# Performance work log

Measured on AMD Instinct MI355X. Metric: run time of the kernel, lower is better.

Reference implementation:

```python
import jax, jax.numpy as jnp
import numpy as np

# per-item cutpoint counts (from np.unique(item_positions, return_counts=True))
NUM_CUTS = np.array([4, 5, 6, 7] * 4)  # 16 items
N_ITEMS = len(NUM_CUTS)
MAX_CP = int(NUM_CUTS.max())  # 7
CP = jnp.asarray(NUM_CUTS)  # [I]
CUT_MASK = jnp.arange(MAX_CP)[None, :] < CP[:, None]  # [I, MAX_CP] valid cutpoints
EPS = 1e-8

B, D_IN, H1, H2 = 65536, 512, 1024, 512


def setup_inputs() -> dict:
    key = jax.random.key(0)
    ks = jax.random.split(key, 10)
    x = jax.random.normal(ks[0], (B, D_IN), dtype=jnp.float32)
    data = jax.random.randint(ks[1], (B, N_ITEMS), 0, 4, dtype=jnp.int64 if jax.config.jax_enable_x64 else jnp.int32)
    W1 = jax.random.normal(ks[2], (D_IN, H1), dtype=jnp.float32) / np.sqrt(D_IN)
    b1 = jnp.zeros((H1,), jnp.float32)
    W2 = jax.random.normal(ks[3], (H1, H2), dtype=jnp.float32) / np.sqrt(H1)
    b2 = jnp.zeros((H2,), jnp.float32)
    Wf = jax.random.normal(ks[4], (H2, N_ITEMS), dtype=jnp.float32) / np.sqrt(H2)
    bf = jnp.zeros((N_ITEMS,), jnp.float32)
    # ragged per-item cutpoint heads padded to MAX_CP (masked in reference)
    Wk = jax.random.normal(ks[5], (N_ITEMS, H2, MAX_CP), dtype=jnp.float32) / np.sqrt(H2)
    bk = jnp.zeros((N_ITEMS, MAX_CP), jnp.float32)
    return {"x": x, "data": data, "W1": W1, "b1": b1, "W2": W2, "b2": b2,
            "Wf": Wf, "bf": bf, "Wk": Wk, "bk": bk}


def reference(x, data, W1, b1, W2, b2, Wf, bf, Wk, bk):
    # trunk MLP: Linear -> ReLU, twice
    h = jax.nn.relu(x @ W1 + b1)
    h = jax.nn.relu(h @ W2 + b2)  # [B, H2]
    f_x = h @ Wf + bf  # [B, I]
    # batched ragged per-item cutpoint heads (padded GEMM + mask)
    cut = jnp.einsum('bh,ihc->bic', h, Wk) + bk  # [B, I, MAX_CP]
    e = jnp.where(CUT_MASK[None], jnp.clip(jnp.exp(cut), EPS, None), 0.0)
    cum = jnp.cumsum(e, axis=-1)  # monotone cutpoints; pads contribute 0
    cum_probs = jnp.clip(jax.nn.sigmoid(cum - f_x[:, :, None]), EPS, 1.0 - EPS)
    # category probs: [cum0, diffs..., 1 - cum_last], ragged lengths cp_i + 1
    diff = jnp.concatenate([cum_probs[..., :1], cum_probs[..., 1:] - cum_probs[..., :-1]], axis=-1)
    last_cum = cum_probs[:, jnp.arange(N_ITEMS), CP - 1]  # [B, I]
    diff_pad = jnp.pad(diff, ((0, 0), (0, 0), (0, 1)))  # [B, I, MAX_CP+1]
    cat = jnp.arange(MAX_CP + 1)[None, None, :]
    probs = jnp.where(cat < CP[None, :, None], diff_pad,
                      jnp.where(cat == CP[None, :, None], (1.0 - last_cum)[:, :, None], 1.0))
    probs = jnp.clip(probs, EPS, 1.0 - EPS)  # [B, I, MAX_CP+1]
    # NLL: gather observed category per (respondent, item)
    gathered = jnp.take_along_axis(probs, data[:, :, None].astype(jnp.int32), axis=2)[..., 0]
    rec_loss = -jnp.log(gathered).mean(axis=0).sum()
    return rec_loss, probs
```

## Files before the change

### kernel.cpp

```cpp
#include <hip/hip_runtime.h>
#include <cmath>

#define EPSV 1e-8f

typedef __bf16 bf16_t;
typedef __bf16 bf16x8 __attribute__((ext_vector_type(8)));
typedef __bf16 bf16x4 __attribute__((ext_vector_type(4)));
typedef float f32x4 __attribute__((ext_vector_type(4)));

__device__ __forceinline__ void gload16(const void* g, void* l) {
    __builtin_amdgcn_global_load_lds(
        (const __attribute__((address_space(1))) void*)g,
        (__attribute__((address_space(3))) void*)l, 16, 0, 0);
}

__device__ __forceinline__ void qmap(int q, int& row, int& u) {
    int prow = q >> 3;
    int v = (q & 7) ^ (prow & 7);
    row = (prow << 1) | (v >> 2);
    u = v & 3;
}
__device__ __forceinline__ int lds_elem(int row, int u) {
    int prow = row >> 1;
    int v = ((row & 1) << 2) | u;
    return prow * 64 + ((v ^ (prow & 7)) << 3);
}

template<bool RELU>
__global__ __launch_bounds__(512, 2) void gemm256(
    const bf16_t* __restrict__ A, const bf16_t* __restrict__ BT,
    const float* __restrict__ bias, bf16_t* __restrict__ C,
    int N, int K, int nbx)
{
    __shared__ bf16_t sm[2][2][2][8192];

    const int t    = threadIdx.x;
    const int lane = t & 63;
    const int w    = t >> 6;
    const int wr   = w >> 2;
    const int wc   = w & 3;
    const int r16  = lane & 15;
    const int u16  = lane >> 4;

    const int nwg = gridDim.x;
    int bid = blockIdx.x;
    int swz = ((nwg & 7) == 0) ? ((bid & 7) * (nwg >> 3) + (bid >> 3)) : bid;
    const int bx = swz % nbx, by = swz / nbx;
    const int m0 = by << 8, n0 = bx << 8;

    int r0, u0, r1, u1;
    qmap(t, r0, u0);
    qmap(t + 512, r1, u1);
    const bf16_t* gA0 = A  + (size_t)(m0 + r0) * K + (u0 << 3);
    const bf16_t* gA1 = A  + (size_t)(m0 + r1) * K + (u1 << 3);
    const bf16_t* gB0 = BT + (size_t)(n0 + r0) * K + (u0 << 3);
    const bf16_t* gB1 = BT + (size_t)(n0 + r1) * K + (u1 << 3);

    auto STAGE = [&](const bf16_t* g0, const bf16_t* g1, bf16_t* sl, int koff) {
        gload16(g0 + koff, sl + (w << 9));
        gload16(g1 + koff, sl + 4096 + (w << 9));
    };

    int aoff[8], boff[4];
#pragma unroll
    for (int i = 0; i < 8; ++i) aoff[i] = lds_elem((wr << 7) + (i << 4) + r16, u16);
#pragma unroll
    for (int j = 0; j < 4; ++j) boff[j] = lds_elem((wc << 6) + (j << 4) + r16, u16);

    f32x4 acc[8][4];
#pragma unroll
    for (int i = 0; i < 8; ++i)
#pragma unroll
        for (int j = 0; j < 4; ++j) acc[i][j] = (f32x4){0.f, 0.f, 0.f, 0.f};

    const int NT = K >> 6;

    STAGE(gA0, gA1, &sm[0][0][0][0], 0);
    STAGE(gB0, gB1, &sm[0][1][0][0], 0);
    STAGE(gA0, gA1, &sm[0][0][1][0], 32);
    STAGE(gB0, gB1, &sm[0][1][1][0], 32);
    STAGE(gA0, gA1, &sm[1][0][0][0], 64);
    STAGE(gB0, gB1, &sm[1][1][0][0], 64);
    asm volatile("s_waitcnt vmcnt(8)" ::: "memory");
    __builtin_amdgcn_s_barrier();

    bf16x8 af0[4], af1[4], bfr[4];
#pragma unroll
    for (int i = 0; i < 4; ++i) af0[i] = *(const bf16x8*)(&sm[0][0][0][0] + aoff[i]);

    for (int kt = 0; kt < NT; ++kt) {
        const int c  = kt & 1;
        const int c1 = c ^ 1;
        const bool s12 = (kt + 1) < NT;
        const bool s34 = (kt + 2) < NT;
        const int k12 = ((kt + 1) << 6) + 32;
        const int k34 = (kt + 2) << 6;
        const bf16_t* sA0 = &sm[c][0][0][0];
        const bf16_t* sA1 = &sm[c][0][1][0];
        const bf16_t* sB0 = &sm[c][1][0][0];
        const bf16_t* sB1 = &sm[c][1][1][0];

#pragma unroll
        for (int j = 0; j < 4; ++j) bfr[j] = *(const bf16x8*)(sB0 + boff[j]);
#pragma unroll
        for (int i = 0; i < 4; ++i) af1[i] = *(const bf16x8*)(sA0 + aoff[4 + i]);
        if (s12) STAGE(gA0, gA1, &sm[c1][0][1][0], k12);
        __builtin_amdgcn_s_barrier();
        __builtin_amdgcn_s_setprio(1);
#pragma unroll
        for (int i = 0; i < 4; ++i)
#pragma unroll
            for (int j = 0; j < 4; ++j)
                acc[i][j] = __builtin_amdgcn_mfma_f32_16x16x32_bf16(bfr[j], af0[i], acc[i][j], 0, 0, 0);
        __builtin_amdgcn_s_setprio(0);
        __builtin_amdgcn_s_barrier();

        if (s12) STAGE(gB0, gB1, &sm[c1][1][1][0], k12);
        if (s12) asm volatile("s_waitcnt vmcnt(8)" ::: "memory");
        else     asm volatile("s_waitcnt vmcnt(0)" ::: "memory");
        __builtin_amdgcn_s_barrier();
#pragma unroll
        for (int i = 0; i < 4; ++i) af0[i] = *(const bf16x8*)(sA1 + aoff[i]);
        __builtin_amdgcn_s_setprio(1);
#pragma unroll
        for (int i = 0; i < 4; ++i)
#pragma unroll
            for (int j = 0; j < 4; ++j)
                acc[4 + i][j] = __builtin_amdgcn_mfma_f32_16x16x32_bf16(bfr[j], af1[i], acc[4 + i][j], 0, 0, 0);
        __builtin_amdgcn_s_setprio(0);
        __builtin_amdgcn_s_barrier();

#pragma unroll
        for (int j = 0; j < 4; ++j) bfr[j] = *(const bf16x8*)(sB1 + boff[j]);
#pragma unroll
        for (int i = 0; i < 4; ++i) af1[i] = *(const bf16x8*)(sA1 + aoff[4 + i]);
        if (s34) STAGE(gA0, gA1, &sm[c][0][0][0], k34);
        __builtin_amdgcn_s_barrier();
        __builtin_amdgcn_s_setprio(1);
#pragma unroll
        for (int i = 0; i < 4; ++i)
#pragma unroll
            for (int j = 0; j < 4; ++j)
                acc[i][j] = __builtin_amdgcn_mfma_f32_16x16x32_bf16(bfr[j], af0[i], acc[i][j], 0, 0, 0);
        __builtin_amdgcn_s_setprio(0);
        __builtin_amdgcn_s_barrier();

        if (s34) STAGE(gB0, gB1, &sm[c][1][0][0], k34);
        if (s34)      asm volatile("s_waitcnt vmcnt(8)" ::: "memory");
        else if (s12) asm volatile("s_waitcnt vmcnt(4)" ::: "memory");
        __builtin_amdgcn_s_barrier();
        if (s12) {
#pragma unroll
            for (int i = 0; i < 4; ++i)
                af0[i] = *(const bf16x8*)(&sm[c1][0][0][0] + aoff[i]);
        }
        __builtin_amdgcn_s_setprio(1);
#pragma unroll
        for (int i = 0; i < 4; ++i)
#pragma unroll
            for (int j = 0; j < 4; ++j)
                acc[4 + i][j] = __builtin_amdgcn_mfma_f32_16x16x32_bf16(bfr[j], af1[i], acc[4 + i][j], 0, 0, 0);
        __builtin_amdgcn_s_setprio(0);
        __builtin_amdgcn_s_barrier();
    }

    __syncthreads();

    char* eb = (char*)&sm[0][0][0][0];
    const int mBb = (wr << 7) + r16;
    const int nBb = (wc << 6) + (u16 << 2);
#pragma unroll
    for (int i = 0; i < 8; ++i) {
        const int m = mBb + (i << 4);
        const int xm = (m & 15) << 4;
#pragma unroll
        for (int j = 0; j < 4; ++j) {
            const int nl = nBb + (j << 4);
            f32x4 bv = *(const f32x4*)(bias + n0 + nl);
            bf16x4 pk;
#pragma unroll
            for (int r = 0; r < 4; ++r) {
                float v = acc[i][j][r] + bv[r];
                if (RELU) v = fmaxf(v, 0.f);
                pk[r] = (bf16_t)v;
            }
            *(bf16x4*)(eb + m * 512 + ((nl << 1) ^ xm)) = pk;
        }
    }
    __syncthreads();
    const int cc = t & 31;
    const int rr = t >> 5;
#pragma unroll
    for (int rp = 0; rp < 16; ++rp) {
        const int m = (rp << 4) + rr;
        bf16x8 v = *(const bf16x8*)(eb + m * 512 + (((cc << 4) ^ ((m & 15) << 4)) & 511));
        *(bf16x8*)(C + (size_t)(m0 + m) * N + n0 + (cc << 3)) = v;
    }
}

__global__ __launch_bounds__(256) void head_fused(
    const bf16_t* __restrict__ A, const bf16_t* __restrict__ BT,
    const float* __restrict__ bias, const int* __restrict__ data,
    float* __restrict__ probs_out, float* __restrict__ partials,
    int K, int row0)
{
    __shared__ __align__(16) bf16_t As[128 * 32];
    __shared__ __align__(16) bf16_t Bs[128 * 32];
    __shared__ float hdl[128 * 128];

    const int t    = threadIdx.x;
    const int lane = t & 63;
    const int w    = t >> 6;
    const int wm   = (w >> 1) << 6;
    const int wn   = (w & 1) << 6;
    const int m0l  = blockIdx.x << 7;

    const int srow  = t >> 2;
    const int skoff = (t & 3) << 3;

    const bf16_t* Ap = A  + (size_t)(m0l + srow) * K + skoff;
    const bf16_t* Bp = BT + (size_t)srow * K + skoff;
    const size_t rstep = (size_t)64 * K;

    bf16_t* lA0 = As + ((w << 6)      ) * 8;
    bf16_t* lA1 = As + ((w << 6) + 256) * 8;
    bf16_t* lB0 = Bs + ((w << 6)      ) * 8;
    bf16_t* lB1 = Bs + ((w << 6) + 256) * 8;

    f32x4 acc[4][4];
#pragma unroll
    for (int i = 0; i < 4; ++i)
#pragma unroll
        for (int j = 0; j < 4; ++j) acc[i][j] = (f32x4){0.f, 0.f, 0.f, 0.f};

    const int r16  = lane & 15;
    const int u16  = lane >> 4;
    const int kblk = u16 << 3;

    for (int k0 = 0; k0 < K; k0 += 32) {
        __syncthreads();
        gload16(Ap + k0,         lA0);
        gload16(Ap + rstep + k0, lA1);
        gload16(Bp + k0,         lB0);
        gload16(Bp + rstep + k0, lB1);
        __syncthreads();

        bf16x8 af[4], bfr[4];
#pragma unroll
        for (int i = 0; i < 4; ++i) {
            af[i]  = *(const bf16x8*)&As[(wm + (i << 4) + r16) * 32 + kblk];
            bfr[i] = *(const bf16x8*)&Bs[(wn + (i << 4) + r16) * 32 + kblk];
        }
#pragma unroll
        for (int i = 0; i < 4; ++i)
#pragma unroll
            for (int j = 0; j < 4; ++j)
                acc[i][j] = __builtin_amdgcn_mfma_f32_16x16x32_bf16(af[i], bfr[j], acc[i][j], 0, 0, 0);
    }

#pragma unroll
    for (int j = 0; j < 4; ++j) {
        const int col = wn + (j << 4) + r16;
        const float bv = bias[col];
#pragma unroll
        for (int i = 0; i < 4; ++i) {
            const int rb = wm + (i << 4) + (u16 << 2);
#pragma unroll
            for (int r = 0; r < 4; ++r)
                hdl[(rb + r) * 128 + col] = acc[i][j][r] + bv;
        }
    }
    __syncthreads();

    float lsum = 0.f;
    const int item = t & 15;
    const int cp   = 4 + (item & 3);
#pragma unroll
    for (int p = 0; p < 8; ++p) {
        const int row = (p << 4) + (t >> 4);
        const float* h = hdl + row * 128;
        const size_t grow = (size_t)row0 + m0l + row;

        const float f = h[item];
        float cumP[7];
        float cum = 0.f;
#pragma unroll
        for (int c = 0; c < 7; ++c) {
            if (c < cp) {
                float e = fmaxf(expf(h[16 + item * 7 + c]), EPSV);
                cum += e;
                float s = 1.f / (1.f + expf(f - cum));
                cumP[c] = fminf(fmaxf(s, EPSV), 1.f - EPSV);
            } else {
                cumP[c] = 0.f;
            }
        }
        float probs[8];
#pragma unroll
        for (int k = 0; k < 8; ++k) {
            float v;
            if (k < cp)       v = (k == 0) ? cumP[0] : (cumP[k] - cumP[k - 1]);
            else if (k == cp) v = 1.f - cumP[cp - 1];
            else              v = 1.f;
            probs[k] = fminf(fmaxf(v, EPSV), 1.f - EPSV);
        }
        float* dst = probs_out + (grow * 16 + item) * 8;
#pragma unroll
        for (int k = 0; k < 8; ++k) dst[k] = probs[k];

        const int d = data[grow * 16 + item];
        float g = probs[0];
#pragma unroll
        for (int k = 1; k < 8; ++k) g = (d == k) ? probs[k] : g;
        lsum += -logf(g);
    }

    __syncthreads();
    float* red = (float*)As;
    red[t] = lsum;
    __syncthreads();
#pragma unroll
    for (int s2 = 128; s2 > 0; s2 >>= 1) {
        if (t < s2) red[t] += red[t + s2];
        __syncthreads();
    }
    if (t == 0) partials[(row0 >> 7) + blockIdx.x] = red[0];
}

__global__ __launch_bounds__(256) void convert_x(
    const float* __restrict__ in, bf16_t* __restrict__ out, int n8)
{
    int i = blockIdx.x * 256 + threadIdx.x;
    if (i >= n8) return;
    const float4* p = (const float4*)in;
    float4 a = p[2 * i], b = p[2 * i + 1];
    bf16x8 v;
    v[0] = (bf16_t)a.x; v[1] = (bf16_t)a.y; v[2] = (bf16_t)a.z; v[3] = (bf16_t)a.w;
    v[4] = (bf16_t)b.x; v[5] = (bf16_t)b.y; v[6] = (bf16_t)b.z; v[7] = (bf16_t)b.w;
    ((bf16x8*)out)[i] = v;
}

__global__ __launch_bounds__(256) void transpose_w(
    const float* __restrict__ in, bf16_t* __restrict__ out,
    int kshift, int N, int total)
{
    int idx = blockIdx.x * 256 + threadIdx.x;
    if (idx >= total) return;
    int n = idx >> kshift;
    int k = idx & ((1 << kshift) - 1);
    out[idx] = (bf16_t)in[(size_t)k * N + n];
}

__global__ __launch_bounds__(256) void pack_head(
    const float* __restrict__ Wf, const float* __restrict__ bfv,
    const float* __restrict__ Wk, const float* __restrict__ bk,
    bf16_t* __restrict__ WhT, float* __restrict__ bhead)
{
    int idx = blockIdx.x * 256 + threadIdx.x;
    int n = idx >> 9;
    int k = idx & 511;
    float v;
    if (n < 16) {
        v = Wf[k * 16 + n];
    } else {
        int m = n - 16;
        int i = m / 7, c = m % 7;
        v = Wk[(size_t)i * 3584 + (size_t)k * 7 + c];
    }
    WhT[idx] = (bf16_t)v;
    if (idx < 128) bhead[idx] = (idx < 16) ? bfv[idx] : bk[idx - 16];
}

__global__ __launch_bounds__(256) void reduce_loss(
    const float* __restrict__ partials, int n, float* __restrict__ out, float scale)
{
    __shared__ float red[256];
    float s = 0.f;
    for (int i = threadIdx.x; i < n; i += 256) s += partials[i];
    red[threadIdx.x] = s;
    __syncthreads();
    for (int k = 128; k > 0; k >>= 1) {
        if (threadIdx.x < k) red[threadIdx.x] += red[threadIdx.x + k];
        __syncthreads();
    }
    if (threadIdx.x == 0) out[0] = red[0] * scale;
}

extern "C" void kernel_launch(void* const* d_in, const int* in_sizes, int n_in,
                              void* d_out, int out_size, void* d_ws, size_t ws_size,
                              hipStream_t stream)
{
    const float* x   = (const float*)d_in[0];
    const int*   dat = (const int*)d_in[1];
    const float* W1  = (const float*)d_in[2];
    const float* b1  = (const float*)d_in[3];
    const float* W2  = (const float*)d_in[4];
    const float* b2  = (const float*)d_in[5];
    const float* Wf  = (const float*)d_in[6];
    const float* bfv = (const float*)d_in[7];
    const float* Wk  = (const float*)d_in[8];
    const float* bk  = (const float*)d_in[9];
    float* out = (float*)d_out;

    const int B = 65536, DIN = 512, H1 = 1024, H2 = 512;

    char* cur = (char*)d_ws;
    auto carve = [&](size_t bytes) {
        char* p = cur;
        cur += (bytes + 255) & ~(size_t)255;
        return p;
    };
    float*  partials = (float*)carve(4096 * 4);
    float*  bhead    = (float*)carve(512);
    bf16_t* W1T      = (bf16_t*)carve((size_t)H1 * DIN * 2);
    bf16_t* W2T      = (bf16_t*)carve((size_t)H2 * H1 * 2);
    bf16_t* WhT      = (bf16_t*)carve((size_t)128 * H2 * 2);

    size_t used = (size_t)(cur - (char*)d_ws);
    size_t avail = (ws_size > used + 1024) ? (ws_size - used - 1024) : 0;
    int SLICE = 2048;
    const int cands[6] = {65536, 32768, 16384, 8192, 4096, 2048};
    for (int ci = 0; ci < 6; ++ci) {
        if ((size_t)cands[ci] * 4096 <= avail) { SLICE = cands[ci]; break; }
    }
    bf16_t* xb = (bf16_t*)carve((size_t)SLICE * DIN * 2);
    bf16_t* h1 = (bf16_t*)carve((size_t)SLICE * H1 * 2);
    bf16_t* h2 = (bf16_t*)carve((size_t)SLICE * H2 * 2);

    transpose_w<<<(H1 * DIN + 255) / 256, 256, 0, stream>>>(W1, W1T, 9,  H1, H1 * DIN);
    transpose_w<<<(H2 * H1 + 255) / 256, 256, 0, stream>>>(W2, W2T, 10, H2, H2 * H1);
    pack_head<<<256, 256, 0, stream>>>(Wf, bfv, Wk, bk, WhT, bhead);

    for (int r0 = 0; r0 < B; r0 += SLICE) {
        convert_x<<<SLICE / 4, 256, 0, stream>>>(x + (size_t)r0 * DIN, xb, SLICE * DIN / 8);
        gemm256<true><<<(SLICE / 256) * (H1 / 256), 512, 0, stream>>>(xb, W1T, b1, h1, H1, DIN, H1 / 256);
        gemm256<true><<<(SLICE / 256) * (H2 / 256), 512, 0, stream>>>(h1, W2T, b2, h2, H2, H1, H2 / 256);
        head_fused<<<SLICE / 128, 256, 0, stream>>>(h2, WhT, bhead, dat, out + 1, partials, H2, r0);
    }
    reduce_loss<<<1, 256, 0, stream>>>(partials, B / 128, out, 1.0f / B);
}
```

Before: 237.5 us.

## Use simpler 128x128 single-buffered GEMM kernel for first layer

```diff
diff --git a/kernel.cpp b/kernel.cpp
--- a/kernel.cpp
+++ b/kernel.cpp
@@ -12,6 +12,103 @@
     __builtin_amdgcn_global_load_lds(
         (const __attribute__((address_space(1))) void*)g,
         (__attribute__((address_space(3))) void*)l, 16, 0, 0);
+}
+
+template<bool RELU>
+__global__ __launch_bounds__(256) void gemm128(
+    const bf16_t* __restrict__ A, const bf16_t* __restrict__ BT,
+    const float* __restrict__ bias, bf16_t* __restrict__ C,
+    int N, int K, int nbx)
+{
+    __shared__ __align__(16) bf16_t As[128 * 32];
+    __shared__ __align__(16) bf16_t Bs[128 * 32];
+    __shared__ __align__(16) char   eb[32768];
+
+    const int t    = threadIdx.x;
+    const int lane = t & 63;
+    const int w    = t >> 6;
+    const int wm   = (w >> 1) << 6;
+    const int wn   = (w & 1) << 6;
+
+    const int nwg = gridDim.x;
+    int bid = blockIdx.x;
+    int swz = ((nwg & 7) == 0) ? ((bid & 7) * (nwg >> 3) + (bid >> 3)) : bid;
+    const int bx = swz % nbx, by = swz / nbx;
+    const int m0 = by << 7, n0 = bx << 7;
+
+    const int srow  = t >> 2;
+    const int skoff = (t & 3) << 3;
+
+    const bf16_t* Ap = A  + (size_t)(m0 + srow) * K + skoff;
+    const bf16_t* Bp = BT + (size_t)(n0 + srow) * K + skoff;
+    const size_t rstep = (size_t)64 * K;
+
+    bf16_t* lA0 = As + ((w << 6)      ) * 8;
+    bf16_t* lA1 = As + ((w << 6) + 256) * 8;
+    bf16_t* lB0 = Bs + ((w << 6)      ) * 8;
+    bf16_t* lB1 = Bs + ((w << 6) + 256) * 8;
+
+    f32x4 acc[4][4];
+#pragma unroll
+    for (int i = 0; i < 4; ++i)
+#pragma unroll
+        for (int j = 0; j < 4; ++j) acc[i][j] = (f32x4){0.f, 0.f, 0.f, 0.f};
+
+    const int r16  = lane & 15;
+    const int u16  = lane >> 4;
+    const int kblk = u16 << 3;
+
+    for (int k0 = 0; k0 < K; k0 += 32) {
+        __syncthreads();
+        gload16(Ap + k0,         lA0);
+        gload16(Ap + rstep + k0, lA1);
+        gload16(Bp + k0,         lB0);
+        gload16(Bp + rstep + k0, lB1);
+        __syncthreads();
+
+        bf16x8 af[4], bfr[4];
+#pragma unroll
+        for (int i = 0; i < 4; ++i) {
+            af[i]  = *(const bf16x8*)&As[(wm + (i << 4) + r16) * 32 + kblk];
+            bfr[i] = *(const bf16x8*)&Bs[(wn + (i << 4) + r16) * 32 + kblk];
+        }
+#pragma unroll
+        for (int i = 0; i < 4; ++i)
+#pragma unroll
+            for (int j = 0; j < 4; ++j)
+                acc[i][j] = __builtin_amdgcn_mfma_f32_16x16x32_bf16(bfr[j], af[i], acc[i][j], 0, 0, 0);
+    }
+
+    __syncthreads();
+
+    const int mBb = wm + r16;
+    const int nBb = wn + (u16 << 2);
+#pragma unroll
+    for (int i = 0; i < 4; ++i) {
+        const int row = mBb + (i << 4);
+        const int xm  = (row & 15) << 4;
+#pragma unroll
+        for (int j = 0; j < 4; ++j) {
+            const int nl = nBb + (j << 4);
+            f32x4 bv = *(const f32x4*)(bias + n0 + nl);
+            bf16x4 pk;
+#pragma unroll
+            for (int r = 0; r < 4; ++r) {
+                float v = acc[i][j][r] + bv[r];
+                if (RELU) v = fmaxf(v, 0.f);
+                pk[r] = (bf16_t)v;
+            }
+            *(bf16x4*)(eb + row * 256 + ((nl << 1) ^ xm)) = pk;
+        }
+    }
+    __syncthreads();
+#pragma unroll
+    for (int rp = 0; rp < 8; ++rp) {
+        const int row = (rp << 4) + (t >> 4);
+        const int c   = t & 15;
+        bf16x8 v = *(const bf16x8*)(eb + row * 256 + ((c << 4) ^ ((row & 15) << 4)));
+        *(bf16x8*)(C + (size_t)(m0 + row) * N + n0 + (c << 3)) = v;
+    }
 }
 
 __device__ __forceinline__ void qmap(int q, int& row, int& u) {
@@ -95,7 +192,6 @@
         const bool s34 = (kt + 2) < NT;
         const int k12 = ((kt + 1) << 6) + 32;
         const int k34 = (kt + 2) << 6;
-        const bf16_t* sA0 = &sm[c][0][0][0];
         const bf16_t* sA1 = &sm[c][0][1][0];
         const bf16_t* sB0 = &sm[c][1][0][0];
         const bf16_t* sB1 = &sm[c][1][1][0];
@@ -103,7 +199,7 @@
 #pragma unroll
         for (int j = 0; j < 4; ++j) bfr[j] = *(const bf16x8*)(sB0 + boff[j]);
 #pragma unroll
-        for (int i = 0; i < 4; ++i) af1[i] = *(const bf16x8*)(sA0 + aoff[4 + i]);
+        for (int i = 0; i < 4; ++i) af1[i] = *(const bf16x8*)(&sm[c][0][0][0] + aoff[4 + i]);
         if (s12) STAGE(gA0, gA1, &sm[c1][0][1][0], k12);
         __builtin_amdgcn_s_barrier();
         __builtin_amdgcn_s_setprio(1);
@@ -433,7 +529,7 @@
 
     for (int r0 = 0; r0 < B; r0 += SLICE) {
         convert_x<<<SLICE / 4, 256, 0, stream>>>(x + (size_t)r0 * DIN, xb, SLICE * DIN / 8);
-        gemm256<true><<<(SLICE / 256) * (H1 / 256), 512, 0, stream>>>(xb, W1T, b1, h1, H1, DIN, H1 / 256);
+        gemm128<true><<<(SLICE / 128) * (H1 / 128), 256, 0, stream>>>(xb, W1T, b1, h1, H1, DIN, H1 / 128);
         gemm256<true><<<(SLICE / 256) * (H2 / 256), 512, 0, stream>>>(h1, W2T, b2, h2, H2, H1, H2 / 256);
         head_fused<<<SLICE / 128, 256, 0, stream>>>(h2, WhT, bhead, dat, out + 1, partials, H2, r0);
     }
```

Result: slower. 282.2 us (+18.8%).

## Fuse fp32-to-bf16 input conversion into first GEMM's A-tile loading

Applied to the files above, without the earlier changes.

```diff
diff --git a/kernel.cpp b/kernel.cpp
--- a/kernel.cpp
+++ b/kernel.cpp
@@ -27,8 +27,8 @@
 }
 
 template<bool RELU>
-__global__ __launch_bounds__(512, 2) void gemm256(
-    const bf16_t* __restrict__ A, const bf16_t* __restrict__ BT,
+__global__ __launch_bounds__(512, 2) void gemm256f(
+    const float* __restrict__ A, const bf16_t* __restrict__ BT,
     const float* __restrict__ bias, bf16_t* __restrict__ C,
     int N, int K, int nbx)
 {
@@ -51,16 +51,36 @@
     int r0, u0, r1, u1;
     qmap(t, r0, u0);
     qmap(t + 512, r1, u1);
-    const bf16_t* gA0 = A  + (size_t)(m0 + r0) * K + (u0 << 3);
-    const bf16_t* gA1 = A  + (size_t)(m0 + r1) * K + (u1 << 3);
+    const float*  gA0 = A  + (size_t)(m0 + r0) * K + (u0 << 3);
+    const float*  gA1 = A  + (size_t)(m0 + r1) * K + (u1 << 3);
     const bf16_t* gB0 = BT + (size_t)(n0 + r0) * K + (u0 << 3);
     const bf16_t* gB1 = BT + (size_t)(n0 + r1) * K + (u1 << 3);
 
-    auto STAGE = [&](const bf16_t* g0, const bf16_t* g1, bf16_t* sl, int koff) {
-        gload16(g0 + koff, sl + (w << 9));
-        gload16(g1 + koff, sl + 4096 + (w << 9));
+    auto STAGE_B = [&](bf16_t* sl, int koff) {
+        gload16(gB0 + koff, sl + (w << 9));
+        gload16(gB1 + koff, sl + 4096 + (w << 9));
     };
 
+    f32x4 ar[2][4];
+    auto LOAD_A = [&](int slot, int koff) {
+        ar[slot][0] = *(const f32x4*)(gA0 + koff);
+        ar[slot][1] = *(const f32x4*)(gA0 + koff + 4);
+        ar[slot][2] = *(const f32x4*)(gA1 + koff);
+        ar[slot][3] = *(const f32x4*)(gA1 + koff + 4);
+    };
+    auto WRITE_A = [&](int slot, bf16_t* sl) {
+        bf16x8 v0, v1;
+#pragma unroll
+        for (int e = 0; e < 4; ++e) {
+            v0[e]     = (bf16_t)ar[slot][0][e];
+            v0[4 + e] = (bf16_t)ar[slot][1][e];
+            v1[e]     = (bf16_t)ar[slot][2][e];
+            v1[4 + e] = (bf16_t)ar[slot][3][e];
+        }
+        *(bf16x8*)(sl + ((size_t)t << 3))         = v0;
+        *(bf16x8*)(sl + ((size_t)(t + 512) << 3)) = v1;
+    };
+
     int aoff[8], boff[4];
 #pragma unroll
     for (int i = 0; i < 8; ++i) aoff[i] = lds_elem((wr << 7) + (i << 4) + r16, u16);
@@ -75,13 +95,17 @@
 
     const int NT = K >> 6;
 
-    STAGE(gA0, gA1, &sm[0][0][0][0], 0);
-    STAGE(gB0, gB1, &sm[0][1][0][0], 0);
-    STAGE(gA0, gA1, &sm[0][0][1][0], 32);
-    STAGE(gB0, gB1, &sm[0][1][1][0], 32);
-    STAGE(gA0, gA1, &sm[1][0][0][0], 64);
-    STAGE(gB0, gB1, &sm[1][1][0][0], 64);
-    asm volatile("s_waitcnt vmcnt(8)" ::: "memory");
+    LOAD_A(0, 0);
+    LOAD_A(1, 32);
+    STAGE_B(&sm[0][1][0][0], 0);
+    STAGE_B(&sm[0][1][1][0], 32);
+    asm volatile("s_waitcnt vmcnt(4)" ::: "memory");
+    WRITE_A(0, &sm[0][0][0][0]);
+    WRITE_A(1, &sm[0][0][1][0]);
+    LOAD_A(0, 64);
+    STAGE_B(&sm[1][1][0][0], 64);
+    asm volatile("s_waitcnt vmcnt(6)" ::: "memory");
+    asm volatile("s_waitcnt lgkmcnt(0)" ::: "memory");
     __builtin_amdgcn_s_barrier();
 
     bf16x8 af0[4], af1[4], bfr[4];
@@ -104,6 +128,185 @@
         for (int j = 0; j < 4; ++j) bfr[j] = *(const bf16x8*)(sB0 + boff[j]);
 #pragma unroll
         for (int i = 0; i < 4; ++i) af1[i] = *(const bf16x8*)(sA0 + aoff[4 + i]);
+        if (s12) LOAD_A(1, k12);
+        __builtin_amdgcn_s_barrier();
+        __builtin_amdgcn_s_setprio(1);
+#pragma unroll
+        for (int i = 0; i < 4; ++i)
+#pragma unroll
+            for (int j = 0; j < 4; ++j)
+                acc[i][j] = __builtin_amdgcn_mfma_f32_16x16x32_bf16(bfr[j], af0[i], acc[i][j], 0, 0, 0);
+        __builtin_amdgcn_s_setprio(0);
+        __builtin_amdgcn_s_barrier();
+
+        if (s12) STAGE_B(&sm[c1][1][1][0], k12);
+        if (s12) asm volatile("s_waitcnt vmcnt(8)" ::: "memory");
+        else     asm volatile("s_waitcnt vmcnt(0)" ::: "memory");
+        __builtin_amdgcn_s_barrier();
+#pragma unroll
+        for (int i = 0; i < 4; ++i) af0[i] = *(const bf16x8*)(sA1 + aoff[i]);
+        __builtin_amdgcn_s_setprio(1);
+#pragma unroll
+        for (int i = 0; i < 4; ++i)
+#pragma unroll
+            for (int j = 0; j < 4; ++j)
+                acc[4 + i][j] = __builtin_amdgcn_mfma_f32_16x16x32_bf16(bfr[j], af1[i], acc[4 + i][j], 0, 0, 0);
+        __builtin_amdgcn_s_setprio(0);
+        if (s12) {
+            WRITE_A(0, &sm[c1][0][0][0]);
+            asm volatile("s_waitcnt lgkmcnt(0)" ::: "memory");
+        }
+        __builtin_amdgcn_s_barrier();
+
+#pragma unroll
+        for (int j = 0; j < 4; ++j) bfr[j] = *(const bf16x8*)(sB1 + boff[j]);
+#pragma unroll
+        for (int i = 0; i < 4; ++i) af1[i] = *(const bf16x8*)(sA1 + aoff[4 + i]);
+        if (s34) LOAD_A(0, k34);
+        __builtin_amdgcn_s_barrier();
+        __builtin_amdgcn_s_setprio(1);
+#pragma unroll
+        for (int i = 0; i < 4; ++i)
+#pragma unroll
+            for (int j = 0; j < 4; ++j)
+                acc[i][j] = __builtin_amdgcn_mfma_f32_16x16x32_bf16(bfr[j], af0[i], acc[i][j], 0, 0, 0);
+        __builtin_amdgcn_s_setprio(0);
+        __builtin_amdgcn_s_barrier();
+
+        if (s34) STAGE_B(&sm[c][1][0][0], k34);
+        if (s34)      asm volatile("s_waitcnt vmcnt(8)" ::: "memory");
+        else if (s12) asm volatile("s_waitcnt vmcnt(2)" ::: "memory");
+        __builtin_amdgcn_s_barrier();
+        if (s12) {
+#pragma unroll
+            for (int i = 0; i < 4; ++i)
+                af0[i] = *(const bf16x8*)(&sm[c1][0][0][0] + aoff[i]);
+        }
+        __builtin_amdgcn_s_setprio(1);
+#pragma unroll
+        for (int i = 0; i < 4; ++i)
+#pragma unroll
+            for (int j = 0; j < 4; ++j)
+                acc[4 + i][j] = __builtin_amdgcn_mfma_f32_16x16x32_bf16(bfr[j], af1[i], acc[4 + i][j], 0, 0, 0);
+        __builtin_amdgcn_s_setprio(0);
+        if (s12) {
+            WRITE_A(1, &sm[c1][0][1][0]);
+            asm volatile("s_waitcnt lgkmcnt(0)" ::: "memory");
+        }
+        __builtin_amdgcn_s_barrier();
+    }
+
+    __syncthreads();
+
+    char* eb = (char*)&sm[0][0][0][0];
+    const int mBb = (wr << 7) + r16;
+    const int nBb = (wc << 6) + (u16 << 2);
+#pragma unroll
+    for (int i = 0; i < 8; ++i) {
+        const int m = mBb + (i << 4);
+        const int xm = (m & 15) << 4;
+#pragma unroll
+        for (int j = 0; j < 4; ++j) {
+            const int nl = nBb + (j << 4);
+            f32x4 bv = *(const f32x4*)(bias + n0 + nl);
+            bf16x4 pk;
+#pragma unroll
+            for (int r = 0; r < 4; ++r) {
+                float v = acc[i][j][r] + bv[r];
+                if (RELU) v = fmaxf(v, 0.f);
+                pk[r] = (bf16_t)v;
+            }
+            *(bf16x4*)(eb + m * 512 + ((nl << 1) ^ xm)) = pk;
+        }
+    }
+    __syncthreads();
+    const int cc = t & 31;
+    const int rr = t >> 5;
+#pragma unroll
+    for (int rp = 0; rp < 16; ++rp) {
+        const int m = (rp << 4) + rr;
+        bf16x8 v = *(const bf16x8*)(eb + m * 512 + (((cc << 4) ^ ((m & 15) << 4)) & 511));
+        *(bf16x8*)(C + (size_t)(m0 + m) * N + n0 + (cc << 3)) = v;
+    }
+}
+
+template<bool RELU>
+__global__ __launch_bounds__(512, 2) void gemm256(
+    const bf16_t* __restrict__ A, const bf16_t* __restrict__ BT,
+    const float* __restrict__ bias, bf16_t* __restrict__ C,
+    int N, int K, int nbx)
+{
+    __shared__ bf16_t sm[2][2][2][8192];
+
+    const int t    = threadIdx.x;
+    const int lane = t & 63;
+    const int w    = t >> 6;
+    const int wr   = w >> 2;
+    const int wc   = w & 3;
+    const int r16  = lane & 15;
+    const int u16  = lane >> 4;
+
+    const int nwg = gridDim.x;
+    int bid = blockIdx.x;
+    int swz = ((nwg & 7) == 0) ? ((bid & 7) * (nwg >> 3) + (bid >> 3)) : bid;
+    const int bx = swz % nbx, by = swz / nbx;
+    const int m0 = by << 8, n0 = bx << 8;
+
+    int r0, u0, r1, u1;
+    qmap(t, r0, u0);
+    qmap(t + 512, r1, u1);
+    const bf16_t* gA0 = A  + (size_t)(m0 + r0) * K + (u0 << 3);
+    const bf16_t* gA1 = A  + (size_t)(m0 + r1) * K + (u1 << 3);
+    const bf16_t* gB0 = BT + (size_t)(n0 + r0) * K + (u0 << 3);
+    const bf16_t* gB1 = BT + (size_t)(n0 + r1) * K + (u1 << 3);
+
+    auto STAGE = [&](const bf16_t* g0, const bf16_t* g1, bf16_t* sl, int koff) {
+        gload16(g0 + koff, sl + (w << 9));
+        gload16(g1 + koff, sl + 4096 + (w << 9));
+    };
+
+    int aoff[8], boff[4];
+#pragma unroll
+    for (int i = 0; i < 8; ++i) aoff[i] = lds_elem((wr << 7) + (i << 4) + r16, u16);
+#pragma unroll
+    for (int j = 0; j < 4; ++j) boff[j] = lds_elem((wc << 6) + (j << 4) + r16, u16);
+
+    f32x4 acc[8][4];
+#pragma unroll
+    for (int i = 0; i < 8; ++i)
+#pragma unroll
+        for (int j = 0; j < 4; ++j) acc[i][j] = (f32x4){0.f, 0.f, 0.f, 0.f};
+
+    const int NT = K >> 6;
+
+    STAGE(gA0, gA1, &sm[0][0][0][0], 0);
+    STAGE(gB0, gB1, &sm[0][1][0][0], 0);
+    STAGE(gA0, gA1, &sm[0][0][1][0], 32);
+    STAGE(gB0, gB1, &sm[0][1][1][0], 32);
+    STAGE(gA0, gA1, &sm[1][0][0][0], 64);
+    STAGE(gB0, gB1, &sm[1][1][0][0], 64);
+    asm volatile("s_waitcnt vmcnt(8)" ::: "memory");
+    __builtin_amdgcn_s_barrier();
+
+    bf16x8 af0[4], af1[4], bfr[4];
+#pragma unroll
+    for (int i = 0; i < 4; ++i) af0[i] = *(const bf16x8*)(&sm[0][0][0][0] + aoff[i]);
+
+    for (int kt = 0; kt < NT; ++kt) {
+        const int c  = kt & 1;
+        const int c1 = c ^ 1;
+        const bool s12 = (kt + 1) < NT;
+        const bool s34 = (kt + 2) < NT;
+        const int k12 = ((kt + 1) << 6) + 32;
+        const int k34 = (kt + 2) << 6;
+        const bf16_t* sA1 = &sm[c][0][1][0];
+        const bf16_t* sB0 = &sm[c][1][0][0];
+        const bf16_t* sB1 = &sm[c][1][1][0];
+
+#pragma unroll
+        for (int j = 0; j < 4; ++j) bfr[j] = *(const bf16x8*)(sB0 + boff[j]);
+#pragma unroll
+        for (int i = 0; i < 4; ++i) af1[i] = *(const bf16x8*)(&sm[c][0][0][0] + aoff[4 + i]);
         if (s12) STAGE(gA0, gA1, &sm[c1][0][1][0], k12);
         __builtin_amdgcn_s_barrier();
         __builtin_amdgcn_s_setprio(1);
@@ -325,19 +528,6 @@
         __syncthreads();
     }
     if (t == 0) partials[(row0 >> 7) + blockIdx.x] = red[0];
-}
-
-__global__ __launch_bounds__(256) void convert_x(
-    const float* __restrict__ in, bf16_t* __restrict__ out, int n8)
-{
-    int i = blockIdx.x * 256 + threadIdx.x;
-    if (i >= n8) return;
-    const float4* p = (const float4*)in;
-    float4 a = p[2 * i], b = p[2 * i + 1];
-    bf16x8 v;
-    v[0] = (bf16_t)a.x; v[1] = (bf16_t)a.y; v[2] = (bf16_t)a.z; v[3] = (bf16_t)a.w;
-    v[4] = (bf16_t)b.x; v[5] = (bf16_t)b.y; v[6] = (bf16_t)b.z; v[7] = (bf16_t)b.w;
-    ((bf16x8*)out)[i] = v;
 }
 
 __global__ __launch_bounds__(256) void transpose_w(
@@ -421,9 +611,8 @@
     int SLICE = 2048;
     const int cands[6] = {65536, 32768, 16384, 8192, 4096, 2048};
     for (int ci = 0; ci < 6; ++ci) {
-        if ((size_t)cands[ci] * 4096 <= avail) { SLICE = cands[ci]; break; }
-    }
-    bf16_t* xb = (bf16_t*)carve((size_t)SLICE * DIN * 2);
+        if ((size_t)cands[ci] * 3072 <= avail) { SLICE = cands[ci]; break; }
+    }
     bf16_t* h1 = (bf16_t*)carve((size_t)SLICE * H1 * 2);
     bf16_t* h2 = (bf16_t*)carve((size_t)SLICE * H2 * 2);
 
@@ -432,9 +621,10 @@
     pack_head<<<256, 256, 0, stream>>>(Wf, bfv, Wk, bk, WhT, bhead);
 
     for (int r0 = 0; r0 < B; r0 += SLICE) {
-        convert_x<<<SLICE / 4, 256, 0, stream>>>(x + (size_t)r0 * DIN, xb, SLICE * DIN / 8);
-        gemm256<true><<<(SLICE / 256) * (H1 / 256), 512, 0, stream>>>(xb, W1T, b1, h1, H1, DIN, H1 / 256);
-        gemm256<true><<<(SLICE / 256) * (H2 / 256), 512, 0, stream>>>(h1, W2T, b2, h2, H2, H1, H2 / 256);
+        gemm256f<true><<<(SLICE / 256) * (H1 / 256), 512, 0, stream>>>(
+            x + (size_t)r0 * DIN, W1T, b1, h1, H1, DIN, H1 / 256);
+        gemm256<true><<<(SLICE / 256) * (H2 / 256), 512, 0, stream>>>(
+            h1, W2T, b2, h2, H2, H1, H2 / 256);
         head_fused<<<SLICE / 128, 256, 0, stream>>>(h2, WhT, bhead, dat, out + 1, partials, H2, r0);
     }
     reduce_loss<<<1, 256, 0, stream>>>(partials, B / 128, out, 1.0f / B);
```

After: 234.7 us. Within noise of the previous version (-1.2%).
